# Optimization experiments

Measured on AMD Instinct MI355X. Metric: run time of the kernel, lower is better.

Reference implementation:

```python
import jax, jax.numpy as jnp
import numpy as np

EPS_PHI = 1e-18  # weight assigned to neighbors outside the support radius


def setup_inputs() -> dict:
    key = jax.random.key(0)
    k1, k2, k3, k4 = jax.random.split(key, 4)
    N, P, K = 2, 100000, 60
    points = jax.random.normal(k1, (N, P, 3), dtype=jnp.float32)
    v = jax.random.normal(k2, (N, P, K, 3), dtype=jnp.float32)
    vn = jax.random.normal(k3, (N, P, K, 3), dtype=jnp.float32)
    # squared support radii: positive, bounded away from zero
    sr = jax.random.uniform(k4, (N, P, K), dtype=jnp.float32) + 0.1
    return {"points": points, "v": v, "vn": vn, "sr": sr}


def reference(points, v, vn, sr):
    # points: (N,P,3); v,vn: (N,P,K,3); sr: (N,P,K)
    p_v = points[:, :, None, :] - v                      # (N,P,K,3)
    dists = jnp.sum(p_v * p_v, axis=-1)                  # (N,P,K) squared distances
    inside = dists < sr                                  # (N,P,K)
    w = 1.0 - dists / sr
    phi_v = jnp.where(inside, (w * w) * (w * w), EPS_PHI)  # quartic kernel weight
    v_to_p_dot_n = jnp.sum(vn * p_v, axis=-1)            # (N,P,K)
    sdf = jnp.sum(phi_v * v_to_p_dot_n, axis=-1) / jnp.sum(phi_v, axis=-1)  # (N,P)
    return jnp.sum(sdf * sdf, axis=-1)                   # (N,)
```

## Files before the change

### kernel.cpp

```cpp
#include <hip/hip_runtime.h>

#define BT  256
#define WPB (BT / 64)
#define RED_THREADS 512
#define EPS_PHI 1e-18f

__global__ __launch_bounds__(BT, 4) void sdf_main60(
    const float* __restrict__ points,
    const float* __restrict__ v,
    const float* __restrict__ vn,
    const float* __restrict__ sr,
    float* __restrict__ ws,
    int P, int nGroups, int nWaves, int slots, int slotStride)
{
    const int lane   = threadIdx.x & 63;
    const int waveId = blockIdx.x * WPB + (threadIdx.x >> 6);
    const int t = lane & 15;
    const int g = lane >> 4;

    const int  i3     = (t < 12) ? (144 + 3 * t) : 177;
    const int  s3i    = (t < 12) ? (48 + t)      : 59;
    const bool valid3 = (t < 12);

    float acc0 = 0.f, acc1 = 0.f;

    for (int grp = waveId; grp < nGroups; grp += nWaves) {
        const int p = grp * 4 + g;
        const float* __restrict__ vrow = v      + (size_t)p * 180;
        const float* __restrict__ nrow = vn     + (size_t)p * 180;
        const float* __restrict__ srow = sr     + (size_t)p * 60;
        const float* __restrict__ prow = points + (size_t)p * 3;
        const int i0 = 3 * t;

        const float vx0 = vrow[i0 +  0], vy0 = vrow[i0 +  1], vz0 = vrow[i0 +  2];
        const float vx1 = vrow[i0 + 48], vy1 = vrow[i0 + 49], vz1 = vrow[i0 + 50];
        const float vx2 = vrow[i0 + 96], vy2 = vrow[i0 + 97], vz2 = vrow[i0 + 98];
        const float vx3 = vrow[i3 +  0], vy3 = vrow[i3 +  1], vz3 = vrow[i3 +  2];
        const float nx0 = nrow[i0 +  0], ny0 = nrow[i0 +  1], nz0 = nrow[i0 +  2];
        const float nx1 = nrow[i0 + 48], ny1 = nrow[i0 + 49], nz1 = nrow[i0 + 50];
        const float nx2 = nrow[i0 + 96], ny2 = nrow[i0 + 97], nz2 = nrow[i0 + 98];
        const float nx3 = nrow[i3 +  0], ny3 = nrow[i3 +  1], nz3 = nrow[i3 +  2];
        const float s0 = srow[t], s1 = srow[t + 16], s2 = srow[t + 32], s3 = srow[s3i];
        const float px = prow[0], py = prow[1], pz = prow[2];

        float num = 0.f, den = 0.f;
        auto body = [&](float vx, float vy, float vz,
                        float nx, float ny, float nz,
                        float s, bool valid) {
            const float dx = px - vx, dy = py - vy, dz = pz - vz;
            const float d2 = dx * dx + dy * dy + dz * dz;
            const float rs = __builtin_amdgcn_rcpf(s);
            const float w  = 1.f - d2 * rs;
            const float w2 = w * w;
            float phi = (d2 < s) ? (w2 * w2) : EPS_PHI;
            if (!valid) phi = 0.f;
            const float dot = nx * dx + ny * dy + nz * dz;
            num += phi * dot;
            den += phi;
        };
        body(vx0, vy0, vz0, nx0, ny0, nz0, s0, true);
        body(vx1, vy1, vz1, nx1, ny1, nz1, s1, true);
        body(vx2, vy2, vz2, nx2, ny2, nz2, s2, true);
        body(vx3, vy3, vz3, nx3, ny3, nz3, s3, valid3);

        #pragma unroll
        for (int off = 1; off <= 8; off <<= 1) {
            num += __shfl_xor(num, off, 64);
            den += __shfl_xor(den, off, 64);
        }

        const float sdf = num * __builtin_amdgcn_rcpf(den);
        const float sq  = sdf * sdf;
        if (t == 0) {
            if (p < P) acc0 += sq; else acc1 += sq;
        }
    }

    #pragma unroll
    for (int off = 1; off <= 32; off <<= 1) {
        acc0 += __shfl_xor(acc0, off, 64);
        acc1 += __shfl_xor(acc1, off, 64);
    }
    if (lane == 0) {
        const int slot = waveId & (slots - 1);
        atomicAdd(&ws[slot * slotStride + 0], acc0);
        atomicAdd(&ws[slot * slotStride + 1], acc1);
    }
}

__global__ void sdf_generic(
    const float* __restrict__ points,
    const float* __restrict__ v,
    const float* __restrict__ vn,
    const float* __restrict__ sr,
    float* __restrict__ ws,
    int NP, int P, int K, int slots, int slotStride)
{
    const int p = blockIdx.x * blockDim.x + threadIdx.x;
    if (p >= NP) return;
    const float px = points[p * 3 + 0];
    const float py = points[p * 3 + 1];
    const float pz = points[p * 3 + 2];
    float num = 0.f, den = 0.f;
    for (int k = 0; k < K; ++k) {
        const size_t b = ((size_t)p * K + k) * 3;
        const float dx = px - v[b + 0];
        const float dy = py - v[b + 1];
        const float dz = pz - v[b + 2];
        const float d2 = dx * dx + dy * dy + dz * dz;
        const float s  = sr[(size_t)p * K + k];
        const float w  = 1.f - d2 / s;
        const float w2 = w * w;
        const float phi = (d2 < s) ? (w2 * w2) : EPS_PHI;
        const float dot = vn[b + 0] * dx + vn[b + 1] * dy + vn[b + 2] * dz;
        num += phi * dot;
        den += phi;
    }
    const float sdf = num / den;
    const int n = p / P;
    const int slot = p & (slots - 1);
    if (n < slotStride) atomicAdd(&ws[slot * slotStride + n], sdf * sdf);
}

__global__ __launch_bounds__(RED_THREADS) void sdf_reduce(
    const float* __restrict__ ws, float* __restrict__ out,
    int N, int slots, int slotStride)
{
    __shared__ float sm0[RED_THREADS];
    __shared__ float sm1[RED_THREADS];
    const int tid = threadIdx.x;
    float a = 0.f, b = 0.f;
    for (int s = tid; s < slots; s += RED_THREADS) {
        a += ws[s * slotStride + 0];
        if (N > 1) b += ws[s * slotStride + 1];
    }
    sm0[tid] = a;
    sm1[tid] = b;
    __syncthreads();
    #pragma unroll
    for (int s = RED_THREADS / 2; s >= 1; s >>= 1) {
        if (tid < s) {
            sm0[tid] += sm0[tid + s];
            sm1[tid] += sm1[tid + s];
        }
        __syncthreads();
    }
    if (tid == 0) {
        out[0] = sm0[0];
        if (N > 1) out[1] = sm1[0];
    }
}

extern "C" void kernel_launch(void* const* d_in, const int* in_sizes, int n_in,
                              void* d_out, int out_size, void* d_ws, size_t ws_size,
                              hipStream_t stream) {
    const float* points = (const float*)d_in[0];
    const float* v      = (const float*)d_in[1];
    const float* vn     = (const float*)d_in[2];
    const float* sr     = (const float*)d_in[3];
    float* out = (float*)d_out;
    float* ws  = (float*)d_ws;

    const int NP = in_sizes[0] / 3;
    const int K  = in_sizes[3] / NP;
    const int N  = out_size;
    const int P  = NP / N;

    int slots = 512, slotStride = 16;
    if (ws_size < (size_t)(slots * slotStride * sizeof(float))) {
        slots = 256; slotStride = 2;
    }

    hipMemsetAsync(ws, 0, (size_t)slots * slotStride * sizeof(float), stream);

    if (K == 60 && (NP & 3) == 0) {
        const int blocks  = 2048;
        const int nWaves  = blocks * WPB;
        const int nGroups = NP / 4;
        sdf_main60<<<blocks, BT, 0, stream>>>(points, v, vn, sr, ws,
                                              P, nGroups, nWaves,
                                              slots, slotStride);
    } else {
        sdf_generic<<<(NP + BT - 1) / BT, BT, 0, stream>>>(
            points, v, vn, sr, ws, NP, P, K, slots, slotStride);
    }
    sdf_reduce<<<1, RED_THREADS, 0, stream>>>(ws, out, N, slots, slotStride);
}
```

Measured before the change: 333.6 us.

## Use float4 vector loads and process two point groups per wave iteration

Each lane now handles four consecutive neighbours through 128-bit float4 loads of v, vn and sr, instead of scalar strided loads. Fifteen of sixteen lanes are active per point. Each wave also processes two groups of four points per iteration, giving more loads in flight. The intent is fewer, wider memory instructions and more memory-level parallelism on a bandwidth-bound kernel, at the cost of one idle lane per sixteen, higher register use, and a requirement that NP be divisible by 8.

```diff
diff --git a/kernel.cpp b/kernel.cpp
--- a/kernel.cpp
+++ b/kernel.cpp
@@ -11,68 +11,76 @@
     const float* __restrict__ vn,
     const float* __restrict__ sr,
     float* __restrict__ ws,
-    int P, int nGroups, int nWaves, int slots, int slotStride)
+    int P, int nPairs, int nWaves, int slots, int slotStride)
 {
     const int lane   = threadIdx.x & 63;
     const int waveId = blockIdx.x * WPB + (threadIdx.x >> 6);
-    const int t = lane & 15;
-    const int g = lane >> 4;
-
-    const int  i3     = (t < 12) ? (144 + 3 * t) : 177;
-    const int  s3i    = (t < 12) ? (48 + t)      : 59;
-    const bool valid3 = (t < 12);
+    const int g  = lane >> 4;
+    const int t  = lane & 15;
+    const int tc = (t < 15) ? t : 14;
+    const bool act = (t < 15);
 
     float acc0 = 0.f, acc1 = 0.f;
 
-    for (int grp = waveId; grp < nGroups; grp += nWaves) {
-        const int p = grp * 4 + g;
-        const float* __restrict__ vrow = v      + (size_t)p * 180;
-        const float* __restrict__ nrow = vn     + (size_t)p * 180;
-        const float* __restrict__ srow = sr     + (size_t)p * 60;
-        const float* __restrict__ prow = points + (size_t)p * 3;
-        const int i0 = 3 * t;
+    for (int pr = waveId; pr < nPairs; pr += nWaves) {
+        const int pA = pr * 8 + g;
+        const int pB = pA + 4;
 
-        const float vx0 = vrow[i0 +  0], vy0 = vrow[i0 +  1], vz0 = vrow[i0 +  2];
-        const float vx1 = vrow[i0 + 48], vy1 = vrow[i0 + 49], vz1 = vrow[i0 + 50];
-        const float vx2 = vrow[i0 + 96], vy2 = vrow[i0 + 97], vz2 = vrow[i0 + 98];
-        const float vx3 = vrow[i3 +  0], vy3 = vrow[i3 +  1], vz3 = vrow[i3 +  2];
-        const float nx0 = nrow[i0 +  0], ny0 = nrow[i0 +  1], nz0 = nrow[i0 +  2];
-        const float nx1 = nrow[i0 + 48], ny1 = nrow[i0 + 49], nz1 = nrow[i0 + 50];
-        const float nx2 = nrow[i0 + 96], ny2 = nrow[i0 + 97], nz2 = nrow[i0 + 98];
-        const float nx3 = nrow[i3 +  0], ny3 = nrow[i3 +  1], nz3 = nrow[i3 +  2];
-        const float s0 = srow[t], s1 = srow[t + 16], s2 = srow[t + 32], s3 = srow[s3i];
-        const float px = prow[0], py = prow[1], pz = prow[2];
+        const float4* vA = (const float4*)(v  + (size_t)pA * 180);
+        const float4* nA = (const float4*)(vn + (size_t)pA * 180);
+        const float4* sA = (const float4*)(sr + (size_t)pA * 60);
+        const float4* vB = (const float4*)(v  + (size_t)pB * 180);
+        const float4* nB = (const float4*)(vn + (size_t)pB * 180);
+        const float4* sB = (const float4*)(sr + (size_t)pB * 60);
 
-        float num = 0.f, den = 0.f;
-        auto body = [&](float vx, float vy, float vz,
-                        float nx, float ny, float nz,
-                        float s, bool valid) {
-            const float dx = px - vx, dy = py - vy, dz = pz - vz;
-            const float d2 = dx * dx + dy * dy + dz * dz;
-            const float rs = __builtin_amdgcn_rcpf(s);
-            const float w  = 1.f - d2 * rs;
-            const float w2 = w * w;
-            float phi = (d2 < s) ? (w2 * w2) : EPS_PHI;
-            if (!valid) phi = 0.f;
-            const float dot = nx * dx + ny * dy + nz * dz;
-            num += phi * dot;
-            den += phi;
+        const float4 av0 = vA[3 * tc + 0], av1 = vA[3 * tc + 1], av2 = vA[3 * tc + 2];
+        const float4 an0 = nA[3 * tc + 0], an1 = nA[3 * tc + 1], an2 = nA[3 * tc + 2];
+        const float4 as4 = sA[tc];
+        const float4 bv0 = vB[3 * tc + 0], bv1 = vB[3 * tc + 1], bv2 = vB[3 * tc + 2];
+        const float4 bn0 = nB[3 * tc + 0], bn1 = nB[3 * tc + 1], bn2 = nB[3 * tc + 2];
+        const float4 bs4 = sB[tc];
+        const float pxA = points[pA * 3 + 0], pyA = points[pA * 3 + 1], pzA = points[pA * 3 + 2];
+        const float pxB = points[pB * 3 + 0], pyB = points[pB * 3 + 1], pzB = points[pB * 3 + 2];
+
+        auto quad = [&](const float4& c0, const float4& c1, const float4& c2,
+                        const float4& m0, const float4& m1, const float4& m2,
+                        const float4& s4, float px, float py, float pz,
+                        float& num, float& den) {
+            auto one = [&](float vx, float vy, float vz,
+                           float nx, float ny, float nz, float s) {
+                const float dx = px - vx, dy = py - vy, dz = pz - vz;
+                const float d2 = dx * dx + dy * dy + dz * dz;
+                const float w  = 1.f - d2 * __builtin_amdgcn_rcpf(s);
+                const float w2 = w * w;
+                float phi = (d2 < s) ? (w2 * w2) : EPS_PHI;
+                if (!act) phi = 0.f;
+                num += phi * (nx * dx + ny * dy + nz * dz);
+                den += phi;
+            };
+            one(c0.x, c0.y, c0.z, m0.x, m0.y, m0.z, s4.x);
+            one(c0.w, c1.x, c1.y, m0.w, m1.x, m1.y, s4.y);
+            one(c1.z, c1.w, c2.x, m1.z, m1.w, m2.x, s4.z);
+            one(c2.y, c2.z, c2.w, m2.y, m2.z, m2.w, s4.w);
         };
-        body(vx0, vy0, vz0, nx0, ny0, nz0, s0, true);
-        body(vx1, vy1, vz1, nx1, ny1, nz1, s1, true);
-        body(vx2, vy2, vz2, nx2, ny2, nz2, s2, true);
-        body(vx3, vy3, vz3, nx3, ny3, nz3, s3, valid3);
+
+        float numA = 0.f, denA = 0.f, numB = 0.f, denB = 0.f;
+        quad(av0, av1, av2, an0, an1, an2, as4, pxA, pyA, pzA, numA, denA);
+        quad(bv0, bv1, bv2, bn0, bn1, bn2, bs4, pxB, pyB, pzB, numB, denB);
 
         #pragma unroll
         for (int off = 1; off <= 8; off <<= 1) {
-            num += __shfl_xor(num, off, 64);
-            den += __shfl_xor(den, off, 64);
+            numA += __shfl_xor(numA, off, 64);
+            denA += __shfl_xor(denA, off, 64);
+            numB += __shfl_xor(numB, off, 64);
+            denB += __shfl_xor(denB, off, 64);
         }
 
-        const float sdf = num * __builtin_amdgcn_rcpf(den);
-        const float sq  = sdf * sdf;
         if (t == 0) {
-            if (p < P) acc0 += sq; else acc1 += sq;
+            const float sdfA = numA * __builtin_amdgcn_rcpf(denA);
+            const float sdfB = numB * __builtin_amdgcn_rcpf(denB);
+            const float sqA = sdfA * sdfA, sqB = sdfB * sdfB;
+            if (pA < P) acc0 += sqA; else acc1 += sqA;
+            if (pB < P) acc0 += sqB; else acc1 += sqB;
         }
     }
 
@@ -173,12 +181,12 @@
 
     hipMemsetAsync(ws, 0, (size_t)slots * slotStride * sizeof(float), stream);
 
-    if (K == 60 && (NP & 3) == 0) {
-        const int blocks  = 2048;
-        const int nWaves  = blocks * WPB;
-        const int nGroups = NP / 4;
+    if (K == 60 && (NP & 7) == 0) {
+        const int blocks = 2048;
+        const int nWaves = blocks * WPB;
+        const int nPairs = NP / 8;
         sdf_main60<<<blocks, BT, 0, stream>>>(points, v, vn, sr, ws,
-                                              P, nGroups, nWaves,
+                                              P, nPairs, nWaves,
                                               slots, slotStride);
     } else {
         sdf_generic<<<(NP + BT - 1) / BT, BT, 0, stream>>>(
```

New measurement: 333.3 us. About the same (-0.1%).
